# Performance work log

Measured on AMD Instinct MI355X. Metric: run time of the kernel, lower is better.

Reference implementation:

```python
import jax, jax.numpy as jnp
import numpy as np

B, S, HID = 4096, 50, 256
NH = 4
HD = HID // NH          # 64
FB = S // 2 + 1         # 26 freq bins
ALPHA = 0.3
LN_EPS = 1e-12


def setup_inputs() -> dict:
    key = jax.random.key(0)
    ks = jax.random.split(key, 10)
    item = jax.random.normal(ks[0], (B, S, HID), dtype=jnp.float32)
    attr = jax.random.normal(ks[1], (B, S, HID), dtype=jnp.float32)
    complex_weight = jax.random.normal(ks[2], (1, NH, S // 2, HD), dtype=jnp.float32) * 0.02
    base_filter = jnp.ones((NH, FB, 1), dtype=jnp.float32)
    base_bias = jnp.full((NH, FB, 1), -0.1, dtype=jnp.float32)
    # adaptive MLP: Linear(HID,HID) -> GELU -> Linear(HID, NH*FB*2)
    w1 = jax.random.normal(ks[3], (HID, HID), dtype=jnp.float32) * (1.0 / np.sqrt(HID))
    b1 = jnp.zeros((HID,), dtype=jnp.float32)
    w2 = jax.random.normal(ks[4], (HID, NH * FB * 2), dtype=jnp.float32) * (1.0 / np.sqrt(HID))
    b2 = jnp.zeros((NH * FB * 2,), dtype=jnp.float32)
    ln_gamma = jnp.ones((HID,), dtype=jnp.float32)
    ln_beta = jnp.zeros((HID,), dtype=jnp.float32)
    return {
        "item_tensor": item, "attr_tensor": attr,
        "complex_weight": complex_weight,
        "base_filter": base_filter, "base_bias": base_bias,
        "w1": w1, "b1": b1, "w2": w2, "b2": b2,
        "ln_gamma": ln_gamma, "ln_beta": ln_beta,
    }


def _forward(item_tensor, attr_tensor, complex_weight, base_filter, base_bias,
             w1, b1, w2, b2, ln_gamma, ln_beta):
    b, s, hid = item_tensor.shape
    # [B, NH, S, HD]
    x_heads = item_tensor.reshape(b, s, NH, HD).transpose(0, 2, 1, 3)

    # ---- frequency branch ----
    F_fft = jnp.fft.rfft(x_heads, axis=2, norm='ortho')  # [B, NH, FB, HD] complex
    attr_ctx = attr_tensor.mean(axis=1)                   # [B, HID]
    h = jax.nn.gelu(attr_ctx @ w1 + b1, approximate=False)
    adapt = (h @ w2 + b2).reshape(b, NH, FB, 2)
    adaptive_scale = adapt[..., 0:1]
    adaptive_bias = adapt[..., 1:2]
    eff_filter = base_filter * (1.0 + adaptive_scale)     # [B, NH, FB, 1]
    eff_bias = base_bias + adaptive_bias                   # real, added to real part
    F_mod = F_fft * eff_filter + eff_bias
    x_fft = jnp.fft.irfft(F_mod, n=s, axis=2, norm='ortho')  # [B, NH, S, HD]

    # ---- Haar wavelet lifting branch (S even => no truncation/pad) ----
    x_even = x_heads[:, :, 0::2, :]
    x_odd = x_heads[:, :, 1::2, :]
    approx = 0.5 * (x_even + x_odd)
    detail = 0.5 * (x_even - x_odd) * complex_weight
    even_recon = approx + detail
    odd_recon = approx - detail
    # interleave even/odd back: [B, NH, S/2, 2, HD] -> [B, NH, S, HD]
    x_wavelet = jnp.stack([even_recon, odd_recon], axis=3).reshape(b, NH, s, HD)

    # ---- gate combine + residual LayerNorm ----
    x_combined = (1.0 - ALPHA) * x_wavelet + ALPHA * x_fft
    x_out = x_combined.transpose(0, 2, 1, 3).reshape(b, s, hid)
    res = x_out + item_tensor  # dropout is identity in eval
    mu = res.mean(axis=-1, keepdims=True)
    var = jnp.mean(jnp.square(res - mu), axis=-1, keepdims=True)
    return (res - mu) * jax.lax.rsqrt(var + LN_EPS) * ln_gamma + ln_beta


def reference(item_tensor, attr_tensor, complex_weight, base_filter, base_bias,
              w1, b1, w2, b2, ln_gamma, ln_beta):
    return _forward(item_tensor, attr_tensor, complex_weight, base_filter, base_bias,
                    w1, b1, w2, b2, ln_gamma, ln_beta)
```

## Files before the change

kernel.cpp:

```cpp
#include <hip/hip_runtime.h>
#include <math.h>
#include <utility>

#define B_    4096
#define S_    50
#define HID_  256
#define NH_   4
#define HD_   64
#define FB_   26
#define NPAIR 25
#define CHUNK 10

__device__ __forceinline__ float rfl_f(float v) {
    union { float f; int i; } u;
    u.f = v;
    u.i = __builtin_amdgcn_readfirstlane(u.i);
    return u.f;
}

__global__ void precompute_kernel(const float* __restrict__ base_filter,
                                  const float* __restrict__ base_bias,
                                  const float* __restrict__ w2,
                                  const float* __restrict__ b2,
                                  float* __restrict__ Wp,
                                  float* __restrict__ C0)
{
    const int m   = blockIdx.x;
    const int j   = threadIdx.x;
    const int h   = m / 100;
    const int rem = m % 100;
    const int cls = rem / 50;
    const int tau = rem % 50;

    const float inv50  = 1.0f / 50.0f;
    const float invs50 = 0.141421356237309515f;

    float acc   = 0.0f;
    float c0acc = 0.0f;
    for (int k = 0; k < FB_; ++k) {
        int   mm   = (k * tau) % 50;
        float cosv = cospif((float)(2 * mm) / 50.0f);
        float wk   = (k == 0 || k == 25) ? 1.0f : 2.0f;
        int   o    = (h * FB_ + k) * 2 + cls;
        float coef;
        if (cls == 0) coef = wk * inv50 * cosv * base_filter[h * FB_ + k];
        else          coef = wk * invs50 * cosv;
        acc += coef * w2[j * 208 + o];
        if (j == 0) {
            if (cls == 0) c0acc += coef * (1.0f + b2[o]);
            else          c0acc += coef * (base_bias[h * FB_ + k] + b2[o]);
        }
    }
    Wp[j * 400 + m] = acc;
    if (j == 0) C0[m] = c0acc;
}

__global__ __launch_bounds__(256)
void mean_kernel(const float* __restrict__ attr, float* __restrict__ ctx)
{
    const int g    = threadIdx.x >> 6;
    const int lane = threadIdx.x & 63;
    const int b    = blockIdx.x * 4 + g;
    const float4* p = (const float4*)(attr + (size_t)b * S_ * HID_) + lane;
    float4 s = make_float4(0.f, 0.f, 0.f, 0.f);
    #pragma unroll
    for (int t = 0; t < S_; ++t) {
        float4 v = p[t * 64];
        s.x += v.x; s.y += v.y; s.z += v.z; s.w += v.w;
    }
    const float is = 1.0f / S_;
    s.x *= is; s.y *= is; s.z *= is; s.w *= is;
    ((float4*)(ctx + (size_t)b * HID_))[lane] = s;
}

template <int EPI>
__global__ __launch_bounds__(256)
void gemm_kernel(const float* __restrict__ A, const float* __restrict__ Bm,
                 const float* __restrict__ bias, float* __restrict__ C,
                 int M, int N, int K)
{
    __shared__ float As[64][33];
    __shared__ float Bs[32][64];
    const int tid = threadIdx.x;
    const int tx = tid & 15, ty = tid >> 4;
    const int col0 = blockIdx.x * 64;
    const int row0 = blockIdx.y * 64;

    float acc[4][4] = {};

    for (int k0 = 0; k0 < K; k0 += 32) {
        #pragma unroll
        for (int l = 0; l < 2; ++l) {
            int f = tid + l * 256;
            int r = f >> 3;
            int c4 = f & 7;
            float4 av = *(const float4*)(A + (size_t)(row0 + r) * K + k0 + c4 * 4);
            As[r][c4 * 4 + 0] = av.x; As[r][c4 * 4 + 1] = av.y;
            As[r][c4 * 4 + 2] = av.z; As[r][c4 * 4 + 3] = av.w;
        }
        #pragma unroll
        for (int l = 0; l < 2; ++l) {
            int f = tid + l * 256;
            int kr = f >> 4;
            int c4 = f & 15;
            int col = col0 + c4 * 4;
            float4 bv = make_float4(0.f, 0.f, 0.f, 0.f);
            if (col < N) bv = *(const float4*)(Bm + (size_t)(k0 + kr) * N + col);
            *(float4*)&Bs[kr][c4 * 4] = bv;
        }
        __syncthreads();
        #pragma unroll
        for (int kk = 0; kk < 32; ++kk) {
            float4 bv = *(float4*)&Bs[kk][tx * 4];
            float br[4] = {bv.x, bv.y, bv.z, bv.w};
            #pragma unroll
            for (int r = 0; r < 4; ++r) {
                float av = As[ty * 4 + r][kk];
                #pragma unroll
                for (int c = 0; c < 4; ++c)
                    acc[r][c] = fmaf(av, br[c], acc[r][c]);
            }
        }
        __syncthreads();
    }

    #pragma unroll
    for (int r = 0; r < 4; ++r) {
        int row = row0 + ty * 4 + r;
        #pragma unroll
        for (int c = 0; c < 4; ++c) {
            int col = col0 + tx * 4 + c;
            if (col < N) {
                float v = acc[r][c] + bias[col];
                if (EPI == 0)
                    v = 0.5f * v * (1.0f + erff(v * 0.70710678118654752f));
                C[(size_t)row * N + col] = v;
            }
        }
    }
}

template <int T, int TP>
__device__ __forceinline__ float cval(const float (&cv)[26]) {
    constexpr int ci = ((T - TP) % 50 + 50) % 50;
    constexpr int dd = (ci > 25) ? (50 - ci) : ci;
    return cv[dd];
}

template <int R0, int TP, int... J>
__device__ __forceinline__ void convJ(float (&a)[CHUNK], const float (&x)[50],
                                      const float (&cv)[26],
                                      std::integer_sequence<int, J...>) {
    ((a[J] = fmaf(cval<R0 + J, TP>(cv), x[TP], a[J])), ...);
}

template <int R0, int... TPs>
__device__ __forceinline__ void convChunk(float (&a)[CHUNK], const float (&x)[50],
                                          const float (&cv)[26],
                                          std::integer_sequence<int, TPs...>) {
    (convJ<R0, TPs>(a, x, cv, std::make_integer_sequence<int, CHUNK>{}), ...);
}

template <int R0>
__device__ __forceinline__ void chunk_proc(const float (&x)[50], const float (&cv)[26],
                                           const float* __restrict__ vb,
                                           const float* __restrict__ cwp,
                                           float gam, float bet,
                                           float* __restrict__ outp,
                                           float (*part)[4][2], int w, int lane)
{
    float a[CHUNK] = {};
    convChunk<R0>(a, x, cv, std::make_integer_sequence<int, 50>{});

    #pragma unroll
    for (int q = 0; q < CHUNK / 2; ++q) {
        const int p = R0 / 2 + q;
        float e  = x[2 * p], o = x[2 * p + 1];
        float ap = 0.5f * (e + o);
        float dt = 0.5f * (e - o) * cwp[p * HD_];
        float ve = rfl_f(vb[2 * p]);
        float vo = rfl_f(vb[2 * p + 1]);
        float fe = a[2 * q]     + ve;
        float fo = a[2 * q + 1] + vo;
        a[2 * q]     = 0.7f * (ap + dt) + 0.3f * fe + e;
        a[2 * q + 1] = 0.7f * (ap - dt) + 0.3f * fo + o;
    }

    float ls = 0.0f, lq = 0.0f;
    #pragma unroll
    for (int j = 0; j < CHUNK; ++j) {
        float s  = a[j];
        float q2 = a[j] * a[j];
        #pragma unroll
        for (int m = 1; m < 64; m <<= 1) {
            s  += __shfl_xor(s,  m, 64);
            q2 += __shfl_xor(q2, m, 64);
        }
        if (lane == j) { ls = s; lq = q2; }
    }
    if (lane < CHUNK) { part[lane][w][0] = ls; part[lane][w][1] = lq; }
    __syncthreads();

    #pragma unroll
    for (int j = 0; j < CHUNK; ++j) {
        float4 pa = *(const float4*)&part[j][0][0];
        float4 pb = *(const float4*)&part[j][2][0];
        float s   = (pa.x + pa.z) + (pb.x + pb.z);
        float qq  = (pa.y + pa.w) + (pb.y + pb.w);
        float mu  = s * (1.0f / HID_);
        float var = qq * (1.0f / HID_) - mu * mu;
        float rs  = rsqrtf(var + 1e-12f);
        outp[(R0 + j) * HID_] = (a[j] - mu) * rs * gam + bet;
    }
}

__global__ __launch_bounds__(256, 4)
void fused_kernel(const float* __restrict__ item,
                  const float* __restrict__ cw,
                  const float* __restrict__ cv,
                  const float* __restrict__ gamma,
                  const float* __restrict__ beta,
                  float* __restrict__ out)
{
    __shared__ float part[5][CHUNK][4][2];

    const int b    = blockIdx.x;
    const int tid  = threadIdx.x;
    const int w    = tid >> 6;
    const int lane = tid & 63;
    const int wu   = __builtin_amdgcn_readfirstlane(w);

    const float* cb = cv + (size_t)b * 400 + wu * 100;
    float cvr[26];
    #pragma unroll
    for (int j = 0; j < 26; ++j)
        cvr[j] = rfl_f(cb[j]);
    const float* vb = cb + 50;

    const float* xp = item + (size_t)b * S_ * HID_ + tid;
    float x[50];
    #pragma unroll
    for (int t = 0; t < 50; ++t) x[t] = xp[t * HID_];

    const float gam = gamma[tid];
    const float bet = beta[tid];
    float* outp = out + (size_t)b * S_ * HID_ + tid;
    const float* cwp = cw + (size_t)(wu * NPAIR) * HD_ + lane;

    chunk_proc< 0>(x, cvr, vb, cwp, gam, bet, outp, part[0], w, lane);
    chunk_proc<10>(x, cvr, vb, cwp, gam, bet, outp, part[1], w, lane);
    chunk_proc<20>(x, cvr, vb, cwp, gam, bet, outp, part[2], w, lane);
    chunk_proc<30>(x, cvr, vb, cwp, gam, bet, outp, part[3], w, lane);
    chunk_proc<40>(x, cvr, vb, cwp, gam, bet, outp, part[4], w, lane);
}

extern "C" void kernel_launch(void* const* d_in, const int* in_sizes, int n_in,
                              void* d_out, int out_size, void* d_ws, size_t ws_size,
                              hipStream_t stream)
{
    (void)in_sizes; (void)n_in; (void)out_size; (void)ws_size;
    const float* item = (const float*)d_in[0];
    const float* attr = (const float*)d_in[1];
    const float* cw   = (const float*)d_in[2];
    const float* bf   = (const float*)d_in[3];
    const float* bb   = (const float*)d_in[4];
    const float* w1   = (const float*)d_in[5];
    const float* b1   = (const float*)d_in[6];
    const float* w2   = (const float*)d_in[7];
    const float* b2   = (const float*)d_in[8];
    const float* g    = (const float*)d_in[9];
    const float* be   = (const float*)d_in[10];
    float* out = (float*)d_out;
    float* ws  = (float*)d_ws;

    float* ctx  = ws;
    float* hbuf = ws + 1048576;
    float* Wp   = ws + 2097152;
    float* C0   = ws + 2199552;
    float* cvb  = ws + 2200064;

    hipLaunchKernelGGL(precompute_kernel, dim3(400), dim3(256), 0, stream,
                       bf, bb, w2, b2, Wp, C0);
    hipLaunchKernelGGL(mean_kernel, dim3(B_ / 4), dim3(256), 0, stream, attr, ctx);
    hipLaunchKernelGGL((gemm_kernel<0>), dim3(4, 64), dim3(256), 0, stream,
                       ctx, w1, b1, hbuf, B_, 256, 256);
    hipLaunchKernelGGL((gemm_kernel<1>), dim3(7, 64), dim3(256), 0, stream,
                       hbuf, Wp, C0, cvb, B_, 400, 256);
    hipLaunchKernelGGL(fused_kernel, dim3(B_), dim3(256), 0, stream,
                       item, cw, cvb, g, be, out);
}
```

Baseline: 668.9 us.

## Reduce LayerNorm rows via shared-memory staging and relax occupancy bound

Each chunk's 10 output rows are written to a shared buffer. Each wave then loads whole rows as float4 and reduces at most 3 of them, where before every wave ran a full 64-lane butterfly for all 10 rows. This removes most of the cross-lane shuffles in the LayerNorm statistics, at the cost of one extra barrier per chunk and more LDS traffic. The launch bound also moves from a minimum of 4 blocks to waves_per_eu(2), which lets the compiler use more registers for the 50-element x array and the accumulators but may lower occupancy.

```diff
diff --git a/kernel.cpp b/kernel.cpp
--- a/kernel.cpp
+++ b/kernel.cpp
@@ -167,7 +167,8 @@
                                            const float* __restrict__ cwp,
                                            float gam, float bet,
                                            float* __restrict__ outp,
-                                           float (*part)[4][2], int w, int lane)
+                                           float (*buf)[HID_], float2* sums,
+                                           int tid, int w, int lane)
 {
     float a[CHUNK] = {};
     convChunk<R0>(a, x, cv, std::make_integer_sequence<int, 50>{});
@@ -178,43 +179,46 @@
         float e  = x[2 * p], o = x[2 * p + 1];
         float ap = 0.5f * (e + o);
         float dt = 0.5f * (e - o) * cwp[p * HD_];
-        float ve = rfl_f(vb[2 * p]);
-        float vo = rfl_f(vb[2 * p + 1]);
-        float fe = a[2 * q]     + ve;
-        float fo = a[2 * q + 1] + vo;
+        float fe = a[2 * q]     + rfl_f(vb[2 * p]);
+        float fo = a[2 * q + 1] + rfl_f(vb[2 * p + 1]);
         a[2 * q]     = 0.7f * (ap + dt) + 0.3f * fe + e;
         a[2 * q + 1] = 0.7f * (ap - dt) + 0.3f * fo + o;
     }
 
-    float ls = 0.0f, lq = 0.0f;
+    #pragma unroll
+    for (int j = 0; j < CHUNK; ++j) buf[j][tid] = a[j];
+    __syncthreads();
+
+    #pragma unroll
+    for (int rr = 0; rr < 3; ++rr) {
+        const int r = w + rr * 4;
+        if (r < CHUNK) {
+            float4 v = *(const float4*)&buf[r][lane * 4];
+            float s  = (v.x + v.y) + (v.z + v.w);
+            float qq = v.x * v.x + v.y * v.y + v.z * v.z + v.w * v.w;
+            #pragma unroll
+            for (int m = 1; m < 64; m <<= 1) {
+                s  += __shfl_xor(s,  m, 64);
+                qq += __shfl_xor(qq, m, 64);
+            }
+            if (lane == 0) {
+                float mu  = s * (1.0f / HID_);
+                float var = qq * (1.0f / HID_) - mu * mu;
+                sums[r] = make_float2(mu, rsqrtf(var + 1e-12f));
+            }
+        }
+    }
+    __syncthreads();
+
     #pragma unroll
     for (int j = 0; j < CHUNK; ++j) {
-        float s  = a[j];
-        float q2 = a[j] * a[j];
-        #pragma unroll
-        for (int m = 1; m < 64; m <<= 1) {
-            s  += __shfl_xor(s,  m, 64);
-            q2 += __shfl_xor(q2, m, 64);
-        }
-        if (lane == j) { ls = s; lq = q2; }
-    }
-    if (lane < CHUNK) { part[lane][w][0] = ls; part[lane][w][1] = lq; }
-    __syncthreads();
-
-    #pragma unroll
-    for (int j = 0; j < CHUNK; ++j) {
-        float4 pa = *(const float4*)&part[j][0][0];
-        float4 pb = *(const float4*)&part[j][2][0];
-        float s   = (pa.x + pa.z) + (pb.x + pb.z);
-        float qq  = (pa.y + pa.w) + (pb.y + pb.w);
-        float mu  = s * (1.0f / HID_);
-        float var = qq * (1.0f / HID_) - mu * mu;
-        float rs  = rsqrtf(var + 1e-12f);
-        outp[(R0 + j) * HID_] = (a[j] - mu) * rs * gam + bet;
-    }
-}
-
-__global__ __launch_bounds__(256, 4)
+        float2 ms = sums[j];
+        outp[(R0 + j) * HID_] = (a[j] - ms.x) * ms.y * gam + bet;
+    }
+}
+
+__global__ __launch_bounds__(256)
+__attribute__((amdgpu_waves_per_eu(2)))
 void fused_kernel(const float* __restrict__ item,
                   const float* __restrict__ cw,
                   const float* __restrict__ cv,
@@ -222,7 +226,8 @@
                   const float* __restrict__ beta,
                   float* __restrict__ out)
 {
-    __shared__ float part[5][CHUNK][4][2];
+    __shared__ float  buf[CHUNK][HID_];
+    __shared__ float2 sums[CHUNK];
 
     const int b    = blockIdx.x;
     const int tid  = threadIdx.x;
@@ -247,11 +252,11 @@
     float* outp = out + (size_t)b * S_ * HID_ + tid;
     const float* cwp = cw + (size_t)(wu * NPAIR) * HD_ + lane;
 
-    chunk_proc< 0>(x, cvr, vb, cwp, gam, bet, outp, part[0], w, lane);
-    chunk_proc<10>(x, cvr, vb, cwp, gam, bet, outp, part[1], w, lane);
-    chunk_proc<20>(x, cvr, vb, cwp, gam, bet, outp, part[2], w, lane);
-    chunk_proc<30>(x, cvr, vb, cwp, gam, bet, outp, part[3], w, lane);
-    chunk_proc<40>(x, cvr, vb, cwp, gam, bet, outp, part[4], w, lane);
+    chunk_proc< 0>(x, cvr, vb, cwp, gam, bet, outp, buf, sums, tid, w, lane);
+    chunk_proc<10>(x, cvr, vb, cwp, gam, bet, outp, buf, sums, tid, w, lane);
+    chunk_proc<20>(x, cvr, vb, cwp, gam, bet, outp, buf, sums, tid, w, lane);
+    chunk_proc<30>(x, cvr, vb, cwp, gam, bet, outp, buf, sums, tid, w, lane);
+    chunk_proc<40>(x, cvr, vb, cwp, gam, bet, outp, buf, sums, tid, w, lane);
 }
 
 extern "C" void kernel_launch(void* const* d_in, const int* in_sizes, int n_in,
```

After: 590.6 us. -11.7%, faster.
